# Kernel tuning notes

Hardware: AMD Instinct MI355X
Metric: run time of the kernel (lower is better)

Reference implementation:

```python
import jax, jax.numpy as jnp
import numpy as np

H_IMG, W_IMG = 32, 32   # img_dim
HID = 256               # hidden_size
B = 128                 # batch


def setup_inputs() -> dict:
    key = jax.random.key(0)
    k1, k2, k3, k4 = jax.random.split(key, 4)
    x = jax.random.normal(k1, (B, H_IMG * W_IMG), dtype=jnp.float32)
    w_ih = jax.random.normal(k2, (4 * HID, 1), dtype=jnp.float32) * 0.1
    w_hh = jax.random.normal(k3, (4 * HID, HID), dtype=jnp.float32) * 0.05
    bias = jax.random.normal(k4, (4 * HID,), dtype=jnp.float32) * 0.1
    return {"x": x, "w_ih": w_ih, "w_hh": w_hh, "bias": bias}


def _mdlstm(x, w_ih, w_hh, bias):
    # x: [B, H*W] in row-major pixel order (pixel_idx = row*W + col)
    Bb = x.shape[0]
    xg = x.reshape(Bb, H_IMG, W_IMG).transpose(1, 2, 0)  # [H, W, B]
    wih_vec = w_ih[:, 0]  # input_size == 1 -> linear is scalar * row-vector

    def cell(x_pix, h_up, s_up, h_left, s_left):
        # Same weight_hh is applied to both directional hidden states; for
        # boundary pixels the corresponding h/s are zeros, so the gating in
        # the original code (skip when row==0 / col==0) holds identically.
        gates = (x_pix[:, None] * wih_vec[None, :]
                 + (h_up + h_left) @ w_hh.T
                 + bias)                                  # [B, 4*HID]
        i, f, g, o = jnp.split(gates, 4, axis=1)
        i = jax.nn.sigmoid(i)
        f = jax.nn.sigmoid(f)
        g = jnp.tanh(g)
        o = jax.nn.sigmoid(o)
        s = f * (s_up + s_left) + i * g                   # shared forgetgate for both dims
        h = o * jnp.tanh(s)
        return h, s

    zeros = jnp.zeros((Bb, HID), x.dtype)

    def row_step(carry, x_row):
        h_up_row, s_up_row = carry                        # [W, B, HID] each

        def col_step(c, inp):
            h_left, s_left = c
            x_pix, h_up, s_up = inp
            h, s = cell(x_pix, h_up, s_up, h_left, s_left)
            return (h, s), (h, s)

        _, (h_row, s_row) = jax.lax.scan(col_step, (zeros, zeros),
                                         (x_row, h_up_row, s_up_row))
        return (h_row, s_row), h_row

    init = (jnp.zeros((W_IMG, Bb, HID), x.dtype),
            jnp.zeros((W_IMG, Bb, HID), x.dtype))
    _, h_all = jax.lax.scan(row_step, init, xg)           # [H, W, B, HID]
    # torch.cat(h_matrix, 1): pixels ordered row-major, each [B, HID]
    return h_all.transpose(2, 0, 1, 3).reshape(Bb, H_IMG * W_IMG * HID)


def reference(x, w_ih, w_hh, bias):
    return _mdlstm(x, w_ih, w_hh, bias)
```

## Files before the change

### kernel.cpp

```cpp
#include <hip/hip_runtime.h>
#include <math.h>


#define HIMG 32
#define WIMG 32
#define BATCH 128
#define HID 256
#define BH (BATCH * HID)
#define SLAB (32 * 128 * 256)

#define PSTR 36

typedef double f64x4 __attribute__((ext_vector_type(4)));

__global__ __launch_bounds__(256, 4)
void mdlstm_diag_kernel(const float* __restrict__ x,
                        const float* __restrict__ wih,
                        const float* __restrict__ whh,
                        const float* __restrict__ bias,
                        float* __restrict__ out,
                        double* __restrict__ hbuf,
                        double* __restrict__ sbuf,
                        int d, int rlo, int nc)
{
    __shared__ double lds[4096];
    double* A_lds = lds;
    float*  W_lds = (float*)(lds + 1024);
    double* G_lds = lds;

    const int tid = threadIdx.x;
    const int id  = blockIdx.x;

    const int rx    = id & 7;
    const int q     = id >> 3;
    const int ktile = q & 7;
    const int ghi   = q >> 3;
    const int g     = ghi * 8 + rx;
    if (g >= nc * 4) return;
    const int cellIdx = g >> 2;
    const int b4      = g & 3;
    const int k0 = ktile * 32;
    const int b0 = b4 * 32;

    const int r = rlo + cellIdx;
    const int c = d - r;
    const int rc = r * WIMG + c;

    const int prev = (d & 1) ^ 1;
    const int cur  = d & 1;
    const double* hp = hbuf + (size_t)prev * SLAB;
    const double* sp = sbuf + (size_t)prev * SLAB;
    double* hc = hbuf + (size_t)cur * SLAB;
    double* sc = sbuf + (size_t)cur * SLAB;

    const bool has_up   = (r > 0);
    const bool has_left = (c > 0);
    const double* hu = hp + (size_t)(r - 1) * BH;
    const double* hl = hp + (size_t)r * BH;

    const int lane = tid & 63;
    const int wid  = tid >> 6;
    const int wb0  = (wid & 1) * 16;
    const int wf0  = (wid >> 1) * 64;
    const int cc   = lane & 15;
    const int gg   = lane >> 4;

    int layout;
    {
        double pa = (cc == 1) ? 1.0 : 0.0;
        double pb = (cc == 2) ? 1.0 : 0.0;
        f64x4 pc = {0.0, 0.0, 0.0, 0.0};
        pc = __builtin_amdgcn_mfma_f64_16x16x4f64(pa, pb, pc, 0, 0, 0);
        double s = fabs(pc[0]) + fabs(pc[1]) + fabs(pc[2]) + fabs(pc[3]);
        #pragma unroll
        for (int off = 32; off > 0; off >>= 1) s += __shfl_xor(s, off, 64);
        unsigned long long h0 = __ballot(lane == 2  && pc[1] == 4.0);
        unsigned long long h1 = __ballot(lane == 18 && pc[0] == 4.0);
        unsigned long long h2 = __ballot(lane == 1  && pc[2] == 4.0);
        unsigned long long h3 = __ballot(lane == 33 && pc[0] == 4.0);
        layout = -1;
        if (s == 4.0) {
            if (h0) layout = 0;
            else if (h1) layout = 1;
            else if (h2) layout = 2;
            else if (h3) layout = 3;
        }
    }
    const bool use_mfma = (layout >= 0);

    const int a_row = tid >> 4;
    const int a_kp  = tid & 15;
    const size_t ga0 = (size_t)(b0 + a_row) * HID + 2 * a_kp;
    const size_t ga1 = ga0 + (size_t)16 * HID;
    const float* w_src[4];
    int w_pos[4];
    #pragma unroll
    for (int p = 0; p < 4; p++) {
        int u = tid + p * 256;
        int phi = u >> 3, kq = u & 7;
        int F = (phi >> 5) * 256 + k0 + (phi & 31);
        w_src[p] = whh + (size_t)F * HID + 4 * kq;
        w_pos[p] = phi * PSTR + 4 * kq;
    }

    f64x4 acc[4];
    #pragma unroll
    for (int ft = 0; ft < 4; ft++) acc[ft] = (f64x4){0.0, 0.0, 0.0, 0.0};

    double2 pu0, pu1, pl0, pl1;
    float4 pw[4];
    {
        const double2 z = {0.0, 0.0};
        pu0 = has_up   ? *(const double2*)(hu + ga0) : z;
        pu1 = has_up   ? *(const double2*)(hu + ga1) : z;
        pl0 = has_left ? *(const double2*)(hl + ga0) : z;
        pl1 = has_left ? *(const double2*)(hl + ga1) : z;
        #pragma unroll
        for (int p = 0; p < 4; p++)
            pw[p] = *(const float4*)(w_src[p]);
    }

    const float* wbase = &W_lds[(wf0 + cc) * PSTR + gg];

    for (int ck = 0; ck < 8; ck++) {
        __syncthreads();
        {
            const int k = 2 * a_kp;
            const double s0x = pu0.x + pl0.x, s0y = pu0.y + pl0.y;
            const double s1x = pu1.x + pl1.x, s1y = pu1.y + pl1.y;
            A_lds[ k      * 32 + ((a_row      + k    ) & 31)] = s0x;
            A_lds[(k + 1) * 32 + ((a_row      + k + 1) & 31)] = s0y;
            A_lds[ k      * 32 + ((a_row + 16 + k    ) & 31)] = s1x;
            A_lds[(k + 1) * 32 + ((a_row + 16 + k + 1) & 31)] = s1y;
        }
        #pragma unroll
        for (int p = 0; p < 4; p++)
            *(float4*)&W_lds[w_pos[p]] = pw[p];
        __syncthreads();

        if (ck < 7) {
            const int kg = (ck + 1) * 32;
            const double2 z = {0.0, 0.0};
            pu0 = has_up   ? *(const double2*)(hu + ga0 + kg) : z;
            pu1 = has_up   ? *(const double2*)(hu + ga1 + kg) : z;
            pl0 = has_left ? *(const double2*)(hl + ga0 + kg) : z;
            pl1 = has_left ? *(const double2*)(hl + ga1 + kg) : z;
            #pragma unroll
            for (int p = 0; p < 4; p++)
                pw[p] = *(const float4*)(w_src[p] + kg);
        }

        if (use_mfma) {
            #pragma unroll
            for (int t = 0; t < 8; t++) {
                const int kq = t * 4 + gg;
                const double aval = A_lds[kq * 32 + ((wb0 + cc + kq) & 31)];
                #pragma unroll
                for (int ft = 0; ft < 4; ft++) {
                    const double bval = (double)wbase[ft * (16 * PSTR) + 4 * t];
                    acc[ft] = __builtin_amdgcn_mfma_f64_16x16x4f64(aval, bval, acc[ft], 0, 0, 0);
                }
            }
        } else {
            for (int k = 0; k < 32; k++) {
                double av[4], wv4[4];
                #pragma unroll
                for (int b = 0; b < 4; b++)
                    av[b] = A_lds[k * 32 + ((wb0 + 4 * gg + b + k) & 31)];
                #pragma unroll
                for (int ft = 0; ft < 4; ft++)
                    wv4[ft] = (double)W_lds[(wf0 + ft * 16 + cc) * PSTR + k];
                #pragma unroll
                for (int ft = 0; ft < 4; ft++)
                    #pragma unroll
                    for (int b = 0; b < 4; b++)
                        acc[ft][b] = fma(av[b], wv4[ft], acc[ft][b]);
            }
        }
    }

    const int ec = tid & 31;
    const int eb = tid >> 5;
    const int kE = k0 + ec;
    double xp4[4], su4[4], sl4[4];
    #pragma unroll
    for (int i = 0; i < 4; i++) {
        const int b = b0 + eb + 8 * i;
        xp4[i] = (double)x[b * (HIMG * WIMG) + rc];
        su4[i] = has_up   ? sp[(size_t)(r - 1) * BH + b * HID + kE] : 0.0;
        sl4[i] = has_left ? sp[(size_t)r * BH + b * HID + kE]       : 0.0;
    }

    __syncthreads();
    const int slay = use_mfma ? layout : 0;
    #pragma unroll
    for (int ft = 0; ft < 4; ft++) {
        #pragma unroll
        for (int b = 0; b < 4; b++) {
            const int rA = (slay & 1) ? (gg + 4 * b) : (4 * gg + b);
            const int m  = (slay >= 2) ? cc : rA;
            const int n  = (slay >= 2) ? rA : cc;
            const int phi  = wf0 + ft * 16 + n;
            const int brow = wb0 + m;
            G_lds[phi * 32 + ((brow + phi) & 31)] = acc[ft][b];
        }
    }
    __syncthreads();

    double wv[4], bv[4];
    #pragma unroll
    for (int g2 = 0; g2 < 4; g2++) {
        wv[g2] = (double)wih[g2 * 256 + kE];
        bv[g2] = (double)bias[g2 * 256 + kE];
    }
    #pragma unroll
    for (int i = 0; i < 4; i++) {
        const int bl = eb + 8 * i;
        const int b = b0 + bl;
        double gate[4];
        #pragma unroll
        for (int g2 = 0; g2 < 4; g2++) {
            const int phi = g2 * 32 + ec;
            gate[g2] = G_lds[phi * 32 + ((bl + phi) & 31)];
        }
        const double gi = gate[0] + xp4[i] * wv[0] + bv[0];
        const double gf = gate[1] + xp4[i] * wv[1] + bv[1];
        const double gG = gate[2] + xp4[i] * wv[2] + bv[2];
        const double go = gate[3] + xp4[i] * wv[3] + bv[3];
        const double iv = 1.0 / (1.0 + exp(-gi));
        const double fv = 1.0 / (1.0 + exp(-gf));
        const double gv = tanh(gG);
        const double ov = 1.0 / (1.0 + exp(-go));
        const double sv = fv * (su4[i] + sl4[i]) + iv * gv;
        const double hv = ov * tanh(sv);
        sc[(size_t)r * BH + b * HID + kE] = sv;
        hc[(size_t)r * BH + b * HID + kE] = hv;
        out[(size_t)b * (HIMG * WIMG * HID) + (size_t)rc * HID + kE] = (float)hv;
    }
}

extern "C" void kernel_launch(void* const* d_in, const int* in_sizes, int n_in,
                              void* d_out, int out_size, void* d_ws, size_t ws_size,
                              hipStream_t stream) {
    const float* x    = (const float*)d_in[0];
    const float* wih  = (const float*)d_in[1];
    const float* whh  = (const float*)d_in[2];
    const float* bias = (const float*)d_in[3];
    float* out = (float*)d_out;

    double* hbuf = (double*)d_ws;
    double* sbuf = hbuf + (size_t)2 * SLAB;

    for (int d = 0; d < HIMG + WIMG - 1; d++) {
        int rlo = d - (WIMG - 1); if (rlo < 0) rlo = 0;
        int rhi = d < (HIMG - 1) ? d : (HIMG - 1);
        int nc = rhi - rlo + 1;
        int g8 = (4 * nc + 7) / 8;
        mdlstm_diag_kernel<<<dim3(g8 * 64), 256, 0, stream>>>(
            x, wih, whh, bias, out, hbuf, sbuf, d, rlo, nc);
    }
}
```

Measured before the change: 3.167 ms.

## Remap MFMA tiles so each thread owns all four gates, drop LDS gate transpose

```diff
diff --git a/kernel.cpp b/kernel.cpp
--- a/kernel.cpp
+++ b/kernel.cpp
@@ -23,10 +23,9 @@
                         double* __restrict__ sbuf,
                         int d, int rlo, int nc)
 {
-    __shared__ double lds[4096];
+    __shared__ double lds[3328];
     double* A_lds = lds;
     float*  W_lds = (float*)(lds + 1024);
-    double* G_lds = lds;
 
     const int tid = threadIdx.x;
     const int id  = blockIdx.x;
@@ -61,7 +60,7 @@
     const int lane = tid & 63;
     const int wid  = tid >> 6;
     const int wb0  = (wid & 1) * 16;
-    const int wf0  = (wid >> 1) * 64;
+    const int wj0  = (wid >> 1) * 16;
     const int cc   = lane & 15;
     const int gg   = lane >> 4;
 
@@ -87,6 +86,7 @@
         }
     }
     const bool use_mfma = (layout >= 0);
+    const int slay = use_mfma ? layout : 0;
 
     const int a_row = tid >> 4;
     const int a_kp  = tid & 15;
@@ -105,7 +105,7 @@
 
     f64x4 acc[4];
     #pragma unroll
-    for (int ft = 0; ft < 4; ft++) acc[ft] = (f64x4){0.0, 0.0, 0.0, 0.0};
+    for (int gt = 0; gt < 4; gt++) acc[gt] = (f64x4){0.0, 0.0, 0.0, 0.0};
 
     double2 pu0, pu1, pl0, pl1;
     float4 pw[4];
@@ -120,7 +120,10 @@
             pw[p] = *(const float4*)(w_src[p]);
     }
 
-    const float* wbase = &W_lds[(wf0 + cc) * PSTR + gg];
+    const float* wbase = &W_lds[(wj0 + cc) * PSTR + gg];
+
+    const int kFast = k0 + wj0 + cc;
+    double xpr[4], sur[4], slr[4];
 
     for (int ck = 0; ck < 8; ck++) {
         __syncthreads();
@@ -148,6 +151,15 @@
             #pragma unroll
             for (int p = 0; p < 4; p++)
                 pw[p] = *(const float4*)(w_src[p] + kg);
+        } else if (slay < 2) {
+            #pragma unroll
+            for (int rg = 0; rg < 4; rg++) {
+                const int m = (slay == 0) ? (4 * gg + rg) : (gg + 4 * rg);
+                const int b = b0 + wb0 + m;
+                xpr[rg] = (double)x[b * (HIMG * WIMG) + rc];
+                sur[rg] = has_up   ? sp[(size_t)(r - 1) * BH + b * HID + kFast] : 0.0;
+                slr[rg] = has_left ? sp[(size_t)r * BH + b * HID + kFast]       : 0.0;
+            }
         }
 
         if (use_mfma) {
@@ -156,86 +168,77 @@
                 const int kq = t * 4 + gg;
                 const double aval = A_lds[kq * 32 + ((wb0 + cc + kq) & 31)];
                 #pragma unroll
-                for (int ft = 0; ft < 4; ft++) {
-                    const double bval = (double)wbase[ft * (16 * PSTR) + 4 * t];
-                    acc[ft] = __builtin_amdgcn_mfma_f64_16x16x4f64(aval, bval, acc[ft], 0, 0, 0);
+                for (int gt = 0; gt < 4; gt++) {
+                    const double bval = (double)wbase[gt * (32 * PSTR) + 4 * t];
+                    acc[gt] = __builtin_amdgcn_mfma_f64_16x16x4f64(aval, bval, acc[gt], 0, 0, 0);
                 }
             }
         } else {
             for (int k = 0; k < 32; k++) {
                 double av[4], wv4[4];
                 #pragma unroll
-                for (int b = 0; b < 4; b++)
-                    av[b] = A_lds[k * 32 + ((wb0 + 4 * gg + b + k) & 31)];
-                #pragma unroll
-                for (int ft = 0; ft < 4; ft++)
-                    wv4[ft] = (double)W_lds[(wf0 + ft * 16 + cc) * PSTR + k];
-                #pragma unroll
-                for (int ft = 0; ft < 4; ft++)
+                for (int rg = 0; rg < 4; rg++)
+                    av[rg] = A_lds[k * 32 + ((wb0 + 4 * gg + rg + k) & 31)];
+                #pragma unroll
+                for (int gt = 0; gt < 4; gt++)
+                    wv4[gt] = (double)W_lds[(gt * 32 + wj0 + cc) * PSTR + k];
+                #pragma unroll
+                for (int gt = 0; gt < 4; gt++)
                     #pragma unroll
-                    for (int b = 0; b < 4; b++)
-                        acc[ft][b] = fma(av[b], wv4[ft], acc[ft][b]);
+                    for (int rg = 0; rg < 4; rg++)
+                        acc[gt][rg] = fma(av[rg], wv4[gt], acc[gt][rg]);
             }
         }
     }
 
-    const int ec = tid & 31;
-    const int eb = tid >> 5;
-    const int kE = k0 + ec;
-    double xp4[4], su4[4], sl4[4];
-    #pragma unroll
-    for (int i = 0; i < 4; i++) {
-        const int b = b0 + eb + 8 * i;
-        xp4[i] = (double)x[b * (HIMG * WIMG) + rc];
-        su4[i] = has_up   ? sp[(size_t)(r - 1) * BH + b * HID + kE] : 0.0;
-        sl4[i] = has_left ? sp[(size_t)r * BH + b * HID + kE]       : 0.0;
-    }
-
-    __syncthreads();
-    const int slay = use_mfma ? layout : 0;
-    #pragma unroll
-    for (int ft = 0; ft < 4; ft++) {
-        #pragma unroll
-        for (int b = 0; b < 4; b++) {
-            const int rA = (slay & 1) ? (gg + 4 * b) : (4 * gg + b);
-            const int m  = (slay >= 2) ? cc : rA;
-            const int n  = (slay >= 2) ? rA : cc;
-            const int phi  = wf0 + ft * 16 + n;
-            const int brow = wb0 + m;
-            G_lds[phi * 32 + ((brow + phi) & 31)] = acc[ft][b];
-        }
-    }
-    __syncthreads();
-
-    double wv[4], bv[4];
-    #pragma unroll
-    for (int g2 = 0; g2 < 4; g2++) {
-        wv[g2] = (double)wih[g2 * 256 + kE];
-        bv[g2] = (double)bias[g2 * 256 + kE];
-    }
-    #pragma unroll
-    for (int i = 0; i < 4; i++) {
-        const int bl = eb + 8 * i;
-        const int b = b0 + bl;
-        double gate[4];
-        #pragma unroll
-        for (int g2 = 0; g2 < 4; g2++) {
-            const int phi = g2 * 32 + ec;
-            gate[g2] = G_lds[phi * 32 + ((bl + phi) & 31)];
-        }
-        const double gi = gate[0] + xp4[i] * wv[0] + bv[0];
-        const double gf = gate[1] + xp4[i] * wv[1] + bv[1];
-        const double gG = gate[2] + xp4[i] * wv[2] + bv[2];
-        const double go = gate[3] + xp4[i] * wv[3] + bv[3];
-        const double iv = 1.0 / (1.0 + exp(-gi));
-        const double fv = 1.0 / (1.0 + exp(-gf));
-        const double gv = tanh(gG);
-        const double ov = 1.0 / (1.0 + exp(-go));
-        const double sv = fv * (su4[i] + sl4[i]) + iv * gv;
-        const double hv = ov * tanh(sv);
-        sc[(size_t)r * BH + b * HID + kE] = sv;
-        hc[(size_t)r * BH + b * HID + kE] = hv;
-        out[(size_t)b * (HIMG * WIMG * HID) + (size_t)rc * HID + kE] = (float)hv;
+    if (slay < 2) {
+        double wv[4], bv[4];
+        #pragma unroll
+        for (int gt = 0; gt < 4; gt++) {
+            wv[gt] = (double)wih[gt * 256 + kFast];
+            bv[gt] = (double)bias[gt * 256 + kFast];
+        }
+        #pragma unroll
+        for (int rg = 0; rg < 4; rg++) {
+            const int m = (slay == 0) ? (4 * gg + rg) : (gg + 4 * rg);
+            const int b = b0 + wb0 + m;
+            const double gi = acc[0][rg] + xpr[rg] * wv[0] + bv[0];
+            const double gf = acc[1][rg] + xpr[rg] * wv[1] + bv[1];
+            const double gG = acc[2][rg] + xpr[rg] * wv[2] + bv[2];
+            const double go = acc[3][rg] + xpr[rg] * wv[3] + bv[3];
+            const double iv = 1.0 / (1.0 + exp(-gi));
+            const double fv = 1.0 / (1.0 + exp(-gf));
+            const double gv = tanh(gG);
+            const double ov = 1.0 / (1.0 + exp(-go));
+            const double sv = fv * (sur[rg] + slr[rg]) + iv * gv;
+            const double hv = ov * tanh(sv);
+            sc[(size_t)r * BH + b * HID + kFast] = sv;
+            hc[(size_t)r * BH + b * HID + kFast] = hv;
+            out[(size_t)b * (HIMG * WIMG * HID) + (size_t)rc * HID + kFast] = (float)hv;
+        }
+    } else {
+        const int b = b0 + wb0 + cc;
+        const double xp = (double)x[b * (HIMG * WIMG) + rc];
+        #pragma unroll
+        for (int rg = 0; rg < 4; rg++) {
+            const int n = (slay == 2) ? (4 * gg + rg) : (gg + 4 * rg);
+            const int kE = k0 + wj0 + n;
+            const double su = has_up   ? sp[(size_t)(r - 1) * BH + b * HID + kE] : 0.0;
+            const double sl = has_left ? sp[(size_t)r * BH + b * HID + kE]       : 0.0;
+            const double gi = acc[0][rg] + xp * (double)wih[0 * 256 + kE] + (double)bias[0 * 256 + kE];
+            const double gf = acc[1][rg] + xp * (double)wih[1 * 256 + kE] + (double)bias[1 * 256 + kE];
+            const double gG = acc[2][rg] + xp * (double)wih[2 * 256 + kE] + (double)bias[2 * 256 + kE];
+            const double go = acc[3][rg] + xp * (double)wih[3 * 256 + kE] + (double)bias[3 * 256 + kE];
+            const double iv = 1.0 / (1.0 + exp(-gi));
+            const double fv = 1.0 / (1.0 + exp(-gf));
+            const double gv = tanh(gG);
+            const double ov = 1.0 / (1.0 + exp(-go));
+            const double sv = fv * (su + sl) + iv * gv;
+            const double hv = ov * tanh(sv);
+            sc[(size_t)r * BH + b * HID + kE] = sv;
+            hc[(size_t)r * BH + b * HID + kE] = hv;
+            out[(size_t)b * (HIMG * WIMG * HID) + (size_t)rc * HID + kE] = (float)hv;
+        }
     }
 }
 
```

New measurement: 3.964 ms. +25.1%, slower.

## Halve per-block batch tile to 16 rows, doubling blocks per diagonal

Applied to the files above, without the earlier changes.

```diff
diff --git a/kernel.cpp b/kernel.cpp
--- a/kernel.cpp
+++ b/kernel.cpp
@@ -9,11 +9,9 @@
 #define BH (BATCH * HID)
 #define SLAB (32 * 128 * 256)
 
-#define PSTR 36
-
 typedef double f64x4 __attribute__((ext_vector_type(4)));
 
-__global__ __launch_bounds__(256, 4)
+__global__ __launch_bounds__(256, 8)
 void mdlstm_diag_kernel(const float* __restrict__ x,
                         const float* __restrict__ wih,
                         const float* __restrict__ whh,
@@ -23,9 +21,9 @@
                         double* __restrict__ sbuf,
                         int d, int rlo, int nc)
 {
-    __shared__ double lds[4096];
+    __shared__ double lds[2560];
     double* A_lds = lds;
-    float*  W_lds = (float*)(lds + 1024);
+    float*  W_lds = (float*)(lds + 512);
     double* G_lds = lds;
 
     const int tid = threadIdx.x;
@@ -36,11 +34,10 @@
     const int ktile = q & 7;
     const int ghi   = q >> 3;
     const int g     = ghi * 8 + rx;
-    if (g >= nc * 4) return;
-    const int cellIdx = g >> 2;
-    const int b4      = g & 3;
+    const int cellIdx = g >> 3;
+    const int bgroup  = g & 7;
     const int k0 = ktile * 32;
-    const int b0 = b4 * 32;
+    const int b0 = bgroup * 16;
 
     const int r = rlo + cellIdx;
     const int c = d - r;
@@ -60,10 +57,10 @@
 
     const int lane = tid & 63;
     const int wid  = tid >> 6;
-    const int wb0  = (wid & 1) * 16;
-    const int wf0  = (wid >> 1) * 64;
+    const int wf0  = wid * 32;
     const int cc   = lane & 15;
     const int gg   = lane >> 4;
+    const int sw   = cc & 7;
 
     int layout;
     {
@@ -91,7 +88,6 @@
     const int a_row = tid >> 4;
     const int a_kp  = tid & 15;
     const size_t ga0 = (size_t)(b0 + a_row) * HID + 2 * a_kp;
-    const size_t ga1 = ga0 + (size_t)16 * HID;
     const float* w_src[4];
     int w_pos[4];
     #pragma unroll
@@ -100,38 +96,35 @@
         int phi = u >> 3, kq = u & 7;
         int F = (phi >> 5) * 256 + k0 + (phi & 31);
         w_src[p] = whh + (size_t)F * HID + 4 * kq;
-        w_pos[p] = phi * PSTR + 4 * kq;
-    }
-
-    f64x4 acc[4];
-    #pragma unroll
-    for (int ft = 0; ft < 4; ft++) acc[ft] = (f64x4){0.0, 0.0, 0.0, 0.0};
-
-    double2 pu0, pu1, pl0, pl1;
+        w_pos[p] = phi * 32 + 4 * (kq ^ (phi & 7));
+    }
+
+    const int ec = tid & 31;
+    const int eb = tid >> 5;
+    const int kE = k0 + ec;
+    double xp2[2], su2[2], sl2[2];
+
+    f64x4 acc[2];
+    acc[0] = (f64x4){0.0, 0.0, 0.0, 0.0};
+    acc[1] = (f64x4){0.0, 0.0, 0.0, 0.0};
+
+    double2 pu0, pl0;
     float4 pw[4];
     {
         const double2 z = {0.0, 0.0};
         pu0 = has_up   ? *(const double2*)(hu + ga0) : z;
-        pu1 = has_up   ? *(const double2*)(hu + ga1) : z;
         pl0 = has_left ? *(const double2*)(hl + ga0) : z;
-        pl1 = has_left ? *(const double2*)(hl + ga1) : z;
         #pragma unroll
         for (int p = 0; p < 4; p++)
             pw[p] = *(const float4*)(w_src[p]);
     }
-
-    const float* wbase = &W_lds[(wf0 + cc) * PSTR + gg];
 
     for (int ck = 0; ck < 8; ck++) {
         __syncthreads();
         {
             const int k = 2 * a_kp;
-            const double s0x = pu0.x + pl0.x, s0y = pu0.y + pl0.y;
-            const double s1x = pu1.x + pl1.x, s1y = pu1.y + pl1.y;
-            A_lds[ k      * 32 + ((a_row      + k    ) & 31)] = s0x;
-            A_lds[(k + 1) * 32 + ((a_row      + k + 1) & 31)] = s0y;
-            A_lds[ k      * 32 + ((a_row + 16 + k    ) & 31)] = s1x;
-            A_lds[(k + 1) * 32 + ((a_row + 16 + k + 1) & 31)] = s1y;
+            A_lds[ k      * 16 + ((a_row + k    ) & 15)] = pu0.x + pl0.x;
+            A_lds[(k + 1) * 16 + ((a_row + k + 1) & 15)] = pu0.y + pl0.y;
         }
         #pragma unroll
         for (int p = 0; p < 4; p++)
@@ -142,67 +135,64 @@
             const int kg = (ck + 1) * 32;
             const double2 z = {0.0, 0.0};
             pu0 = has_up   ? *(const double2*)(hu + ga0 + kg) : z;
-            pu1 = has_up   ? *(const double2*)(hu + ga1 + kg) : z;
             pl0 = has_left ? *(const double2*)(hl + ga0 + kg) : z;
-            pl1 = has_left ? *(const double2*)(hl + ga1 + kg) : z;
             #pragma unroll
             for (int p = 0; p < 4; p++)
                 pw[p] = *(const float4*)(w_src[p] + kg);
+        } else {
+            #pragma unroll
+            for (int i = 0; i < 2; i++) {
+                const int b = b0 + eb + 8 * i;
+                xp2[i] = (double)x[b * (HIMG * WIMG) + rc];
+                su2[i] = has_up   ? sp[(size_t)(r - 1) * BH + b * HID + kE] : 0.0;
+                sl2[i] = has_left ? sp[(size_t)r * BH + b * HID + kE]       : 0.0;
+            }
         }
 
         if (use_mfma) {
             #pragma unroll
             for (int t = 0; t < 8; t++) {
                 const int kq = t * 4 + gg;
-                const double aval = A_lds[kq * 32 + ((wb0 + cc + kq) & 31)];
+                const double aval = A_lds[kq * 16 + ((cc + kq) & 15)];
                 #pragma unroll
-                for (int ft = 0; ft < 4; ft++) {
-                    const double bval = (double)wbase[ft * (16 * PSTR) + 4 * t];
+                for (int ft = 0; ft < 2; ft++) {
+                    const int phi = wf0 + ft * 16 + cc;
+                    const double bval =
+                        (double)W_lds[phi * 32 + 4 * (t ^ sw) + gg];
                     acc[ft] = __builtin_amdgcn_mfma_f64_16x16x4f64(aval, bval, acc[ft], 0, 0, 0);
                 }
             }
         } else {
             for (int k = 0; k < 32; k++) {
-                double av[4], wv4[4];
+                const int kg2 = k >> 2, ke = k & 3;
+                double av[4];
                 #pragma unroll
-                for (int b = 0; b < 4; b++)
-                    av[b] = A_lds[k * 32 + ((wb0 + 4 * gg + b + k) & 31)];
+                for (int rg = 0; rg < 4; rg++)
+                    av[rg] = A_lds[k * 16 + ((4 * gg + rg + k) & 15)];
                 #pragma unroll
-                for (int ft = 0; ft < 4; ft++)
-                    wv4[ft] = (double)W_lds[(wf0 + ft * 16 + cc) * PSTR + k];
-                #pragma unroll
-                for (int ft = 0; ft < 4; ft++)
+                for (int ft = 0; ft < 2; ft++) {
+                    const int phi = wf0 + ft * 16 + cc;
+                    const double wv =
+                        (double)W_lds[phi * 32 + 4 * (kg2 ^ (phi & 7)) + ke];
                     #pragma unroll
-                    for (int b = 0; b < 4; b++)
-                        acc[ft][b] = fma(av[b], wv4[ft], acc[ft][b]);
+                    for (int rg = 0; rg < 4; rg++)
+                        acc[ft][rg] = fma(av[rg], wv, acc[ft][rg]);
+                }
             }
         }
-    }
-
-    const int ec = tid & 31;
-    const int eb = tid >> 5;
-    const int kE = k0 + ec;
-    double xp4[4], su4[4], sl4[4];
-    #pragma unroll
-    for (int i = 0; i < 4; i++) {
-        const int b = b0 + eb + 8 * i;
-        xp4[i] = (double)x[b * (HIMG * WIMG) + rc];
-        su4[i] = has_up   ? sp[(size_t)(r - 1) * BH + b * HID + kE] : 0.0;
-        sl4[i] = has_left ? sp[(size_t)r * BH + b * HID + kE]       : 0.0;
     }
 
     __syncthreads();
     const int slay = use_mfma ? layout : 0;
     #pragma unroll
-    for (int ft = 0; ft < 4; ft++) {
+    for (int ft = 0; ft < 2; ft++) {
         #pragma unroll
         for (int b = 0; b < 4; b++) {
             const int rA = (slay & 1) ? (gg + 4 * b) : (4 * gg + b);
             const int m  = (slay >= 2) ? cc : rA;
             const int n  = (slay >= 2) ? rA : cc;
-            const int phi  = wf0 + ft * 16 + n;
-            const int brow = wb0 + m;
-            G_lds[phi * 32 + ((brow + phi) & 31)] = acc[ft][b];
+            const int phi = wf0 + ft * 16 + n;
+            G_lds[phi * 16 + ((m + phi) & 15)] = acc[ft][b];
         }
     }
     __syncthreads();
@@ -214,24 +204,24 @@
         bv[g2] = (double)bias[g2 * 256 + kE];
     }
     #pragma unroll
-    for (int i = 0; i < 4; i++) {
+    for (int i = 0; i < 2; i++) {
         const int bl = eb + 8 * i;
         const int b = b0 + bl;
         double gate[4];
         #pragma unroll
         for (int g2 = 0; g2 < 4; g2++) {
             const int phi = g2 * 32 + ec;
-            gate[g2] = G_lds[phi * 32 + ((bl + phi) & 31)];
-        }
-        const double gi = gate[0] + xp4[i] * wv[0] + bv[0];
-        const double gf = gate[1] + xp4[i] * wv[1] + bv[1];
-        const double gG = gate[2] + xp4[i] * wv[2] + bv[2];
-        const double go = gate[3] + xp4[i] * wv[3] + bv[3];
+            gate[g2] = G_lds[phi * 16 + ((bl + phi) & 15)];
+        }
+        const double gi = gate[0] + xp2[i] * wv[0] + bv[0];
+        const double gf = gate[1] + xp2[i] * wv[1] + bv[1];
+        const double gG = gate[2] + xp2[i] * wv[2] + bv[2];
+        const double go = gate[3] + xp2[i] * wv[3] + bv[3];
         const double iv = 1.0 / (1.0 + exp(-gi));
         const double fv = 1.0 / (1.0 + exp(-gf));
         const double gv = tanh(gG);
         const double ov = 1.0 / (1.0 + exp(-go));
-        const double sv = fv * (su4[i] + sl4[i]) + iv * gv;
+        const double sv = fv * (su2[i] + sl2[i]) + iv * gv;
         const double hv = ov * tanh(sv);
         sc[(size_t)r * BH + b * HID + kE] = sv;
         hc[(size_t)r * BH + b * HID + kE] = hv;
@@ -255,8 +245,7 @@
         int rlo = d - (WIMG - 1); if (rlo < 0) rlo = 0;
         int rhi = d < (HIMG - 1) ? d : (HIMG - 1);
         int nc = rhi - rlo + 1;
-        int g8 = (4 * nc + 7) / 8;
-        mdlstm_diag_kernel<<<dim3(g8 * 64), 256, 0, stream>>>(
+        mdlstm_diag_kernel<<<dim3(nc * 64), 256, 0, stream>>>(
             x, wih, whh, bias, out, hbuf, sbuf, d, rlo, nc);
     }
 }
```

New measurement: 6.238 ms. 1.97x slower.
